# Kernel optimization log

Measured on AMD Instinct MI355X. Metric: run time of the kernel, lower is better.

## Reference

```python
import jax, jax.numpy as jnp
import numpy as np

N = 100_000          # nodes
DEG = 16             # avg degree (random edges)
E = N * DEG + N      # edges incl. self-loops (ensures no zero in-degree)
NFEAT = 256
NHID = 64
NHEADS = 8
NCLASS = 40
NEG_SLOPE = 0.2
S_F = 1.0
EPS = 1e-6


def setup_inputs() -> dict:
    key = jax.random.key(0)
    ks = jax.random.split(key, 12)
    x = jax.random.normal(ks[0], (N, NFEAT), dtype=jnp.float32)
    loops = jnp.arange(N, dtype=jnp.int32)
    src = jnp.concatenate([jax.random.randint(ks[1], (N * DEG,), 0, N, dtype=jnp.int32), loops])
    dst = jnp.concatenate([jax.random.randint(ks[2], (N * DEG,), 0, N, dtype=jnp.int32), loops])
    # layer-1: NHEADS independent single-head GATConv_G(nfeat -> nhid)
    W1 = (jax.random.normal(ks[3], (NHEADS, NHID, NFEAT), dtype=jnp.float32) * 0.05)
    al1 = jax.random.normal(ks[4], (NHEADS, NHID), dtype=jnp.float32) * 0.05
    ar1 = jax.random.normal(ks[5], (NHEADS, NHID), dtype=jnp.float32) * 0.05
    b1 = jnp.zeros((NHEADS, NHID), dtype=jnp.float32)
    p1 = jax.random.normal(ks[6], (NHEADS,), dtype=jnp.float32) * 0.1
    # layer-2: single-head GATConv_G(nhid*nheads -> nclass)
    W2 = jax.random.normal(ks[7], (NCLASS, NHID * NHEADS), dtype=jnp.float32) * 0.05
    al2 = jax.random.normal(ks[8], (NCLASS,), dtype=jnp.float32) * 0.05
    ar2 = jax.random.normal(ks[9], (NCLASS,), dtype=jnp.float32) * 0.05
    b2 = jnp.zeros((NCLASS,), dtype=jnp.float32)
    p2 = jax.random.normal(ks[10], (), dtype=jnp.float32) * 0.1
    return dict(x=x, src=src, dst=dst, W1=W1, al1=al1, ar1=ar1, b1=b1, p1=p1,
                W2=W2, al2=al2, ar2=ar2, b2=b2, p2=p2)


def _leaky_relu(x):
    return jnp.where(x >= 0, x, NEG_SLOPE * x)


def _edge_softmax(e, dst):
    # softmax over incoming edges of each destination node
    m = jax.ops.segment_max(e, dst, num_segments=N)
    ex = jnp.exp(e - m[dst])
    s = jax.ops.segment_sum(ex, dst, num_segments=N)
    return ex / s[dst]


def _gat_g_head(x, src, dst, W, al, ar, b, p):
    """One GATConv_G with num_heads=1. x:[N,Fin], W:[Fout,Fin] -> [N,Fout]."""
    ft = x @ W.T                                   # [N,Fout]
    el = ft @ al                                   # [N]
    er = ft @ ar                                   # [N]
    e = _leaky_relu(el[src] + er[dst])             # [E]
    a = _edge_softmax(e, dst)                      # [E]
    pe = jax.nn.sigmoid(p) + S_F                   # scalar, nonlinear-aggregation exponent
    mu = ft.min()                                  # global min (shift to make base positive)
    pf = jnp.power(ft - mu + EPS, pe)              # [N,Fout]
    msg = pf[src] * a[:, None]                     # [E,Fout] (u_mul_e)
    agg = jax.ops.segment_sum(msg, dst, num_segments=N)   # sum aggregation
    rst = jnp.power(agg + EPS, 1.0 / pe) + mu      # generalized-mean inverse
    return rst + b                                 # bias [Fout]


def reference(x, src, dst, W1, al1, ar1, b1, p1, W2, al2, ar2, b2, p2):
    # layer 1: NHEADS single-head GATConv_G, each with concat=True => elu, then concat
    heads = []
    for h in range(NHEADS):  # small fixed loop over structurally distinct heads
        heads.append(jax.nn.elu(_gat_g_head(x, src, dst, W1[h], al1[h], ar1[h], b1[h], p1[h])))
    hcat = jnp.concatenate(heads, axis=-1)         # [N, NHEADS*NHID]
    # layer 2: output GATConv_G (concat=False), then log_softmax classifier head
    out = _gat_g_head(hcat, src, dst, W2, al2, ar2, b2, p2)   # [N, NCLASS]
    return jax.nn.log_softmax(out, axis=-1)
```

## Files before the change

### kernel.cpp

```cpp
#include <hip/hip_runtime.h>

#define NN 100000
#define EE 1700000
#define F1 256
#define NH 8
#define HF 64
#define C1 512
#define C2 40
#define EPS 1e-6f

#define OF_PF1   ((size_t)0)
#define OF_HCAT  (OF_PF1  + 102400000ULL)
#define OF_FT2   (OF_HCAT + 102400000ULL)
#define OF_EL1   (OF_FT2  + 16000000ULL)
#define OF_ER1   (OF_EL1  + 3200000ULL)
#define OF_EL2   (OF_ER1  + 3200000ULL)
#define OF_ER2   (OF_EL2  + 400000ULL)
#define OF_DEG   (OF_ER2  + 400000ULL)
#define OF_OFFS  (OF_DEG  + 400000ULL)
#define OF_CUR   (OF_OFFS + 400128ULL)
#define OF_SRCC  (OF_CUR  + 400000ULL)
#define OF_BSUM  (OF_SRCC + 6800000ULL)
#define OF_BOFF  (OF_BSUM + 2048ULL)
#define OF_PRM   (OF_BOFF + 2048ULL)
#define OF_XH    (OF_HCAT)
#define OF_WH    (OF_HCAT + 51200000ULL)


typedef _Float16 f16x8 __attribute__((ext_vector_type(8)));
typedef _Float16 f16x4 __attribute__((ext_vector_type(4)));
typedef float f32x4 __attribute__((ext_vector_type(4)));

__device__ __forceinline__ unsigned f2key(float f){
  unsigned u = __float_as_uint(f);
  return (u & 0x80000000u) ? ~u : (u | 0x80000000u);
}
__device__ __forceinline__ float key2f(unsigned k){
  unsigned u = (k & 0x80000000u) ? (k & 0x7FFFFFFFu) : ~k;
  return __uint_as_float(u);
}
__device__ __forceinline__ unsigned short f2b(float f){
  unsigned u = __float_as_uint(f);
  unsigned r = u + 0x7FFFu + ((u >> 16) & 1u);
  return (unsigned short)(r >> 16);
}
__device__ __forceinline__ float b2f(unsigned short b){
  return __uint_as_float(((unsigned)b) << 16);
}
__device__ __forceinline__ float leaky(float e){ return e >= 0.f ? e : 0.2f*e; }

__device__ __forceinline__ void gload16(const _Float16* g, char* l){
  __builtin_amdgcn_global_load_lds((const __attribute__((address_space(1))) void*)g,
                                   (__attribute__((address_space(3))) void*)l, 16, 0, 0);
}

__global__ void k_init(const float* __restrict__ p1, const float* __restrict__ p2, unsigned* __restrict__ prm){
  int t = threadIdx.x;
  float* prf = (float*)prm;
  if (t < 8){
    prm[t] = 0xFFFFFFFFu;
    float pe = 1.f/(1.f + __expf(-p1[t])) + 1.0f;
    prf[16 + t] = pe;
    prf[24 + t] = 1.f/pe;
  }
  if (t == 0){
    prm[8] = 0xFFFFFFFFu;
    float pe = 1.f/(1.f + __expf(-p2[0])) + 1.0f;
    prf[32] = pe;
    prf[33] = 1.f/pe;
  }
}

__global__ void k_zero_deg(int* __restrict__ deg){
  int i = blockIdx.x*256 + threadIdx.x;
  if (i < NN) deg[i] = 0;
}

__global__ void k_cvt16(const float* __restrict__ in, _Float16* __restrict__ out){
  int i = blockIdx.x*256 + threadIdx.x;
  const float4* p = (const float4*)in + (size_t)i*2;
  float4 a = p[0], b = p[1];
  f16x8 h = {(_Float16)a.x,(_Float16)a.y,(_Float16)a.z,(_Float16)a.w,
             (_Float16)b.x,(_Float16)b.y,(_Float16)b.z,(_Float16)b.w};
  *((f16x8*)out + i) = h;
}

#define G1_BM 128
#define G1_BN 128
#define G1_BK 64
__global__ __launch_bounds__(256) void k_gemm1(const _Float16* __restrict__ xh, const _Float16* __restrict__ Wh,
                                               unsigned short* __restrict__ ft1b, unsigned* __restrict__ prm){
  __shared__ __align__(16) char smem[35840];
  char* Abase = smem;
  char* Bbase = smem + 16384;
  unsigned short (*Cs)[136] = (unsigned short (*)[136])smem;

  int t = threadIdx.x;
  int lane = t & 63, w = t >> 6;
  int wr = w >> 1, wc = w & 1;
  int ct = blockIdx.x * G1_BN;
  int rt = blockIdx.y * G1_BM;

  int lr8 = lane >> 3;
  int gcs = (lane & 7) ^ lr8;

  f32x4 zero = {0.f,0.f,0.f,0.f};
  f32x4 acc[4][4];
  #pragma unroll
  for (int m=0;m<4;m++)
    #pragma unroll
    for (int n=0;n<4;n++) acc[m][n] = zero;

  for (int kt = 0; kt < F1; kt += G1_BK){
    #pragma unroll
    for (int i = 0; i < 4; i++){
      int ch = w*4 + i;
      int row = ch*8 + lr8;
      int ga = min(rt + row, NN-1);
      gload16(xh + (size_t)ga*F1 + kt + gcs*8, Abase + ch*1024);
      gload16(Wh + (size_t)(ct+row)*F1 + kt + gcs*8, Bbase + ch*1024);
    }
    __syncthreads();
    #pragma unroll
    for (int kk = 0; kk < 2; kk++){
      f16x8 af[4], bf[4];
      #pragma unroll
      for (int m=0;m<4;m++){
        int row = wr*64 + m*16 + (lane & 15);
        int g = kk*4 + (lane >> 4);
        af[m] = *(f16x8*)(Abase + ((row*8 + (g ^ (row & 7)))<<4));
      }
      #pragma unroll
      for (int n=0;n<4;n++){
        int row = wc*64 + n*16 + (lane & 15);
        int g = kk*4 + (lane >> 4);
        bf[n] = *(f16x8*)(Bbase + ((row*8 + (g ^ (row & 7)))<<4));
      }
      #pragma unroll
      for (int m=0;m<4;m++)
        #pragma unroll
        for (int n=0;n<4;n++)
          acc[m][n] = __builtin_amdgcn_mfma_f32_16x16x32_f16(af[m], bf[n], acc[m][n], 0, 0, 0);
    }
    __syncthreads();
  }

  int h = (ct >> 6) + wc;
  unsigned kmin = 0xFFFFFFFFu;
  #pragma unroll
  for (int m=0;m<4;m++){
    #pragma unroll
    for (int n=0;n<4;n++){
      int cl = wc*64 + n*16 + (lane & 15);
      int rl = wr*64 + m*16 + (lane >> 4)*4;
      #pragma unroll
      for (int j=0;j<4;j++){
        unsigned short ub = f2b(acc[m][n][j]);
        Cs[rl + j][cl] = ub;
        kmin = min(kmin, f2key(b2f(ub)));
      }
    }
  }
  #pragma unroll
  for (int off=1; off<64; off<<=1) kmin = min(kmin, (unsigned)__shfl_xor((int)kmin, off));
  if (lane == 0) atomicMin(&prm[h], kmin);
  __syncthreads();

  #pragma unroll
  for (int p = 0; p < 8; p++){
    int flat = p*256 + t;
    int row = flat >> 4;
    int q   = flat & 15;
    int gr = rt + row;
    if (gr < NN){
      uint4 v = *(const uint4*)&Cs[row][q*8];
      *(uint4*)&ft1b[(size_t)gr*C1 + ct + q*8] = v;
    }
  }
}

__global__ void k_count(const int* __restrict__ dst, int* __restrict__ deg){
  int e = blockIdx.x*256 + threadIdx.x;
  if (e < EE) atomicAdd(&deg[dst[e]], 1);
}
__global__ void k_scan1(const int* __restrict__ deg, int* __restrict__ offs, int* __restrict__ bsum){
  __shared__ int s[256];
  int t = threadIdx.x; int i = blockIdx.x*256 + t;
  int v = (i < NN) ? deg[i] : 0;
  s[t] = v; __syncthreads();
  for (int off=1; off<256; off<<=1){
    int tmp = (t>=off) ? s[t-off] : 0;
    __syncthreads(); s[t] += tmp; __syncthreads();
  }
  if (i < NN) offs[i] = s[t] - v;
  if (t == 255) bsum[blockIdx.x] = s[255];
}
__global__ void k_scan2(int* __restrict__ bsum, int* __restrict__ boff, int nb){
  __shared__ int s[512];
  int t = threadIdx.x;
  int v = (t < nb) ? bsum[t] : 0;
  s[t] = v; __syncthreads();
  for (int off=1; off<512; off<<=1){
    int tmp = (t>=off) ? s[t-off] : 0;
    __syncthreads(); s[t] += tmp; __syncthreads();
  }
  if (t < nb) boff[t] = s[t] - v;
}
__global__ void k_scan3(int* __restrict__ offs, int* __restrict__ cur, const int* __restrict__ boff){
  int i = blockIdx.x*256 + threadIdx.x;
  if (i < NN){
    int v = offs[i] + boff[blockIdx.x];
    offs[i] = v; cur[i] = v;
  }
  if (i == 0) offs[NN] = EE;
}
__global__ void k_fill(const int* __restrict__ src, const int* __restrict__ dst,
                       int* __restrict__ cur, int* __restrict__ srcc){
  int e = blockIdx.x*256 + threadIdx.x;
  if (e < EE){
    int d = dst[e];
    int pos = atomicAdd(&cur[d], 1);
    srcc[pos] = src[e];
  }
}

__global__ __launch_bounds__(256) void k_transform1(unsigned short* __restrict__ ft1b,
    const float* __restrict__ al1, const float* __restrict__ ar1,
    float* __restrict__ el1, float* __restrict__ er1, const unsigned* __restrict__ prm){
  int lane = threadIdx.x & 63; int w = threadIdx.x >> 6;
  int n = blockIdx.x*4 + w;
  if (n >= NN) return;
  const float* prf = (const float*)prm;
  float vv[8], elp[8], erp[8];
  #pragma unroll
  for (int h=0; h<8; h++){
    vv[h]  = b2f(ft1b[(size_t)n*C1 + h*HF + lane]);
    elp[h] = vv[h]*al1[h*HF + lane];
    erp[h] = vv[h]*ar1[h*HF + lane];
  }
  #pragma unroll
  for (int h=0; h<8; h++){
    #pragma unroll
    for (int off=1; off<64; off<<=1){
      elp[h] += __shfl_xor(elp[h], off);
      erp[h] += __shfl_xor(erp[h], off);
    }
  }
  if (lane == 0){
    #pragma unroll
    for (int h=0; h<8; h++){ el1[(size_t)n*8+h]=elp[h]; er1[(size_t)n*8+h]=erp[h]; }
  }
  #pragma unroll
  for (int h=0; h<8; h++){
    float mu = key2f(prm[h]);
    float pe = prf[16+h];
    float base = vv[h] - mu + EPS;
    ft1b[(size_t)n*C1 + h*HF + lane] = f2b(__expf(pe * __logf(base)));
  }
}

__global__ __launch_bounds__(256) void k_agg1(const unsigned short* __restrict__ pf1b,
    const float* __restrict__ el1, const float* __restrict__ er1,
    const int* __restrict__ offs, const int* __restrict__ srcc,
    const float* __restrict__ b1, const unsigned* __restrict__ prm,
    _Float16* __restrict__ hcath){
  int lane = threadIdx.x & 63; int w = threadIdx.x >> 6;
  int v = blockIdx.x*4 + w;
  if (v >= NN) return;
  const float* prf = (const float*)prm;
  int h = lane >> 3;
  int s = lane & 7;
  int start = offs[v], end = offs[v+1];
  float erh = er1[(size_t)v*8 + h];

  float m = -INFINITY;
  for (int pos = start + s; pos < end; pos += 8){
    int u = srcc[pos];
    float e = leaky(el1[(size_t)u*8 + h] + erh);
    m = fmaxf(m, e);
  }
  m = fmaxf(m, __shfl_xor(m,1)); m = fmaxf(m, __shfl_xor(m,2)); m = fmaxf(m, __shfl_xor(m,4));
  float S = 0.f;
  for (int pos = start + s; pos < end; pos += 8){
    int u = srcc[pos];
    float e = leaky(el1[(size_t)u*8 + h] + erh);
    S += __expf(e - m);
  }
  S += __shfl_xor(S,1); S += __shfl_xor(S,2); S += __shfl_xor(S,4);
  float invS = 1.f / S;

  int es = lane >> 5;
  int hc = (lane >> 2) & 7;
  int q4 = lane & 3;
  float mh    = __shfl(m,    hc*8);
  float invSh = __shfl(invS, hc*8);
  float erhc  = __shfl(erh,  hc*8);

  float acc[16];
  #pragma unroll
  for (int j=0;j<16;j++) acc[j]=0.f;
  for (int pos = start + es; pos < end; pos += 2){
    int u = srcc[pos];
    float e = leaky(el1[(size_t)u*8 + hc] + erhc);
    float a = __expf(e - mh) * invSh;
    const unsigned short* pr = &pf1b[(size_t)u*C1 + hc*HF + q4*16];
    uint4 qa = *(const uint4*)pr;
    uint4 qb = *(const uint4*)(pr + 8);
    acc[0]  += a*b2f((unsigned short)(qa.x & 0xFFFFu));
    acc[1]  += a*b2f((unsigned short)(qa.x >> 16));
    acc[2]  += a*b2f((unsigned short)(qa.y & 0xFFFFu));
    acc[3]  += a*b2f((unsigned short)(qa.y >> 16));
    acc[4]  += a*b2f((unsigned short)(qa.z & 0xFFFFu));
    acc[5]  += a*b2f((unsigned short)(qa.z >> 16));
    acc[6]  += a*b2f((unsigned short)(qa.w & 0xFFFFu));
    acc[7]  += a*b2f((unsigned short)(qa.w >> 16));
    acc[8]  += a*b2f((unsigned short)(qb.x & 0xFFFFu));
    acc[9]  += a*b2f((unsigned short)(qb.x >> 16));
    acc[10] += a*b2f((unsigned short)(qb.y & 0xFFFFu));
    acc[11] += a*b2f((unsigned short)(qb.y >> 16));
    acc[12] += a*b2f((unsigned short)(qb.z & 0xFFFFu));
    acc[13] += a*b2f((unsigned short)(qb.z >> 16));
    acc[14] += a*b2f((unsigned short)(qb.w & 0xFFFFu));
    acc[15] += a*b2f((unsigned short)(qb.w >> 16));
  }
  #pragma unroll
  for (int j=0;j<16;j++) acc[j] += __shfl_xor(acc[j], 32);

  float mu = key2f(prm[hc]);
  float ipe = prf[24+hc];
  int fb = q4*16 + es*8;
  f16x8 o;
  #pragma unroll
  for (int j=0;j<8;j++){
    float r = __expf(ipe * __logf(acc[es*8 + j] + EPS)) + mu + b1[hc*HF + fb + j];
    o[j] = (_Float16)((r > 0.f) ? r : (__expf(r) - 1.f));
  }
  *(f16x8*)&hcath[(size_t)v*C1 + hc*HF + fb] = o;
}

#define G2_BM 64
#define G2_BK 64
__global__ __launch_bounds__(256) void k_gemm2(const _Float16* __restrict__ hcath, const float* __restrict__ W2,
    float* __restrict__ ft2, float* __restrict__ el2, float* __restrict__ er2,
    const float* __restrict__ al2, const float* __restrict__ ar2, unsigned* __restrict__ prm){
  __shared__ float As[G2_BK][G2_BM];
  __shared__ float Bs[G2_BK][C2];
  __shared__ float els[64], ers[64];
  __shared__ unsigned mk;
  int t = threadIdx.x;
  int tx = t & 7, ty = t >> 3;
  int rt = blockIdx.x * G2_BM;
  float acc[2][5];
  #pragma unroll
  for (int i=0;i<2;i++)
    #pragma unroll
    for (int j=0;j<5;j++) acc[i][j]=0.f;

  for (int k0=0; k0<C1; k0+=G2_BK){
    #pragma unroll
    for (int i=0;i<2;i++){
      int id = t*2 + i;
      int row = id >> 3; int c8 = (id & 7)*8;
      int gr = rt + row;
      f16x8 q = {0,0,0,0,0,0,0,0};
      if (gr < NN) q = *(const f16x8*)&hcath[(size_t)gr*C1 + k0 + c8];
      #pragma unroll
      for (int j=0;j<8;j++) As[c8+j][row] = (float)q[j];
    }
    #pragma unroll
    for (int i=0;i<10;i++){
      int id = t + i*256;
      int c = id >> 6, kk = id & 63;
      Bs[kk][c] = W2[(size_t)c*C1 + k0 + kk];
    }
    __syncthreads();
    #pragma unroll
    for (int kk=0; kk<G2_BK; ++kk){
      float2 a = *(float2*)&As[kk][ty*2];
      float b0=Bs[kk][tx*5+0], b1v=Bs[kk][tx*5+1], b2v=Bs[kk][tx*5+2], b3v=Bs[kk][tx*5+3], b4v=Bs[kk][tx*5+4];
      acc[0][0]+=a.x*b0; acc[0][1]+=a.x*b1v; acc[0][2]+=a.x*b2v; acc[0][3]+=a.x*b3v; acc[0][4]+=a.x*b4v;
      acc[1][0]+=a.y*b0; acc[1][1]+=a.y*b1v; acc[1][2]+=a.y*b2v; acc[1][3]+=a.y*b3v; acc[1][4]+=a.y*b4v;
    }
    __syncthreads();
  }

  if (t < 64){ els[t]=0.f; ers[t]=0.f; }
  if (t == 0) mk = 0xFFFFFFFFu;
  __syncthreads();
  unsigned kmin = 0xFFFFFFFFu;
  #pragma unroll
  for (int i=0;i<2;i++){
    int r = rt + ty*2 + i;
    if (r < NN){
      float elp=0.f, erp=0.f;
      #pragma unroll
      for (int j=0;j<5;j++){
        float vv = acc[i][j]; int c = tx*5+j;
        ft2[(size_t)r*C2 + c] = vv;
        elp += vv*al2[c]; erp += vv*ar2[c];
        kmin = min(kmin, f2key(vv));
      }
      atomicAdd(&els[ty*2+i], elp);
      atomicAdd(&ers[ty*2+i], erp);
    }
  }
  atomicMin(&mk, kmin);
  __syncthreads();
  if (t < 64 && rt + t < NN){ el2[rt+t]=els[t]; er2[rt+t]=ers[t]; }
  if (t == 0) atomicMin(&prm[8], mk);
}

__global__ void k_transform2(float* __restrict__ ft2, const unsigned* __restrict__ prm){
  int i = blockIdx.x*256 + threadIdx.x;
  if (i >= NN*C2) return;
  const float* prf = (const float*)prm;
  float mu = key2f(prm[8]);
  float pe = prf[32];
  float v = ft2[i];
  ft2[i] = __expf(pe * __logf(v - mu + EPS));
}

__global__ __launch_bounds__(256) void k_agg2(const float* __restrict__ pf2,
    const float* __restrict__ el2, const float* __restrict__ er2,
    const int* __restrict__ offs, const int* __restrict__ srcc,
    const float* __restrict__ b2, const unsigned* __restrict__ prm,
    float* __restrict__ out){
  int lane = threadIdx.x & 63; int w = threadIdx.x >> 6;
  int v = blockIdx.x*4 + w;
  if (v >= NN) return;
  const float* prf = (const float*)prm;
  int start = offs[v], end = offs[v+1];
  float erv = er2[v];

  float m = -INFINITY;
  for (int pos = start + lane; pos < end; pos += 64){
    float e = leaky(el2[srcc[pos]] + erv);
    m = fmaxf(m, e);
  }
  #pragma unroll
  for (int off=1; off<64; off<<=1) m = fmaxf(m, __shfl_xor(m, off));
  float S = 0.f;
  for (int pos = start + lane; pos < end; pos += 64){
    float e = leaky(el2[srcc[pos]] + erv);
    S += __expf(e - m);
  }
  #pragma unroll
  for (int off=1; off<64; off<<=1) S += __shfl_xor(S, off);
  float invS = 1.f / S;

  int s = lane >> 4;
  int c = lane & 15;
  float a0=0.f, a1=0.f, a2=0.f, a3=0.f;
  for (int pos = start + s; pos < end; pos += 4){
    int u = srcc[pos];
    float a = __expf(leaky(el2[u] + erv) - m) * invS;
    if (c < 10){
      float4 q = *(const float4*)&pf2[(size_t)u*C2 + c*4];
      a0 += a*q.x; a1 += a*q.y; a2 += a*q.z; a3 += a*q.w;
    }
  }
  a0 += __shfl_xor(a0,16); a1 += __shfl_xor(a1,16); a2 += __shfl_xor(a2,16); a3 += __shfl_xor(a3,16);
  a0 += __shfl_xor(a0,32); a1 += __shfl_xor(a1,32); a2 += __shfl_xor(a2,32); a3 += __shfl_xor(a3,32);

  float y[4];
  float mx;
  if (c < 10){
    float mu = key2f(prm[8]);
    float ipe = prf[33];
    float av[4] = {a0,a1,a2,a3};
    #pragma unroll
    for (int j=0;j<4;j++) y[j] = __expf(ipe * __logf(av[j] + EPS)) + mu + b2[c*4 + j];
    mx = fmaxf(fmaxf(y[0],y[1]), fmaxf(y[2],y[3]));
  } else {
    y[0]=y[1]=y[2]=y[3]=-INFINITY;
    mx = -INFINITY;
  }
  mx = fmaxf(mx, __shfl_xor(mx,1)); mx = fmaxf(mx, __shfl_xor(mx,2));
  mx = fmaxf(mx, __shfl_xor(mx,4)); mx = fmaxf(mx, __shfl_xor(mx,8));
  float se = 0.f;
  if (c < 10){
    #pragma unroll
    for (int j=0;j<4;j++) se += __expf(y[j] - mx);
  }
  se += __shfl_xor(se,1); se += __shfl_xor(se,2); se += __shfl_xor(se,4); se += __shfl_xor(se,8);
  float ls = __logf(se);
  if (s == 0 && c < 10){
    float4 o = make_float4(y[0]-mx-ls, y[1]-mx-ls, y[2]-mx-ls, y[3]-mx-ls);
    *(float4*)&out[(size_t)v*C2 + c*4] = o;
  }
}

extern "C" void kernel_launch(void* const* d_in, const int* in_sizes, int n_in,
                              void* d_out, int out_size, void* d_ws, size_t ws_size,
                              hipStream_t stream){
  const float* x   = (const float*)d_in[0];
  const int*   src = (const int*)d_in[1];
  const int*   dst = (const int*)d_in[2];
  const float* W1  = (const float*)d_in[3];
  const float* al1 = (const float*)d_in[4];
  const float* ar1 = (const float*)d_in[5];
  const float* b1  = (const float*)d_in[6];
  const float* p1  = (const float*)d_in[7];
  const float* W2  = (const float*)d_in[8];
  const float* al2 = (const float*)d_in[9];
  const float* ar2 = (const float*)d_in[10];
  const float* b2  = (const float*)d_in[11];
  const float* p2  = (const float*)d_in[12];
  float* out = (float*)d_out;
  char* ws = (char*)d_ws;

  unsigned short* pf1b  = (unsigned short*)(ws + OF_PF1);
  _Float16* hcath = (_Float16*)(ws + OF_HCAT);
  _Float16* xh  = (_Float16*)(ws + OF_XH);
  _Float16* Wh  = (_Float16*)(ws + OF_WH);
  float* ft2   = (float*)(ws + OF_FT2);
  float* el1   = (float*)(ws + OF_EL1);
  float* er1   = (float*)(ws + OF_ER1);
  float* el2   = (float*)(ws + OF_EL2);
  float* er2   = (float*)(ws + OF_ER2);
  int*   deg   = (int*)(ws + OF_DEG);
  int*   offs  = (int*)(ws + OF_OFFS);
  int*   cur   = (int*)(ws + OF_CUR);
  int*   srcc  = (int*)(ws + OF_SRCC);
  int*   bsum  = (int*)(ws + OF_BSUM);
  int*   boff  = (int*)(ws + OF_BOFF);
  unsigned* prm = (unsigned*)(ws + OF_PRM);

  const int NB1 = (NN + 255)/256;
  const int NBE = (EE + 255)/256;

  k_init<<<1, 64, 0, stream>>>(p1, p2, prm);
  k_zero_deg<<<NB1, 256, 0, stream>>>(deg);
  k_cvt16<<<12500, 256, 0, stream>>>(x, xh);
  k_cvt16<<<64, 256, 0, stream>>>(W1, Wh);
  k_gemm1<<<dim3(C1/G1_BN, (NN + G1_BM - 1)/G1_BM), 256, 0, stream>>>(xh, Wh, pf1b, prm);
  k_count<<<NBE, 256, 0, stream>>>(dst, deg);
  k_scan1<<<NB1, 256, 0, stream>>>(deg, offs, bsum);
  k_scan2<<<1, 512, 0, stream>>>(bsum, boff, NB1);
  k_scan3<<<NB1, 256, 0, stream>>>(offs, cur, boff);
  k_fill<<<NBE, 256, 0, stream>>>(src, dst, cur, srcc);
  k_transform1<<<NN/4, 256, 0, stream>>>(pf1b, al1, ar1, el1, er1, prm);
  k_agg1<<<NN/4, 256, 0, stream>>>(pf1b, el1, er1, offs, srcc, b1, prm, hcath);
  k_gemm2<<<(NN + G2_BM - 1)/G2_BM, 256, 0, stream>>>(hcath, W2, ft2, el2, er2, al2, ar2, prm);
  k_transform2<<<(NN*C2 + 255)/256, 256, 0, stream>>>(ft2, prm);
  k_agg2<<<NN/4, 256, 0, stream>>>(ft2, el2, er2, offs, srcc, b2, prm, out);
}
```

Before: 1.014 ms.

## Rewrite layer-2 GEMM with fp16 MFMA and swizzled LDS tiles

Replaces the scalar fp32 FMA layer-2 GEMM (hcat x W2^T) with an MFMA 16x16x32 f16 kernel on 128-row tiles. W2 is padded to 48 rows and converted to fp16 by a new small kernel. Operand tiles are loaded into LDS with an XOR swizzle to avoid bank conflicts. The el/er reductions move from LDS atomics to wave shuffles. The aim is to cut the compute-bound cost of the second GEMM, at the price of fp16 rounding on W2 and one extra launch.

```diff
diff --git a/kernel.cpp b/kernel.cpp
--- a/kernel.cpp
+++ b/kernel.cpp
@@ -23,6 +23,7 @@
 #define OF_BSUM  (OF_SRCC + 6800000ULL)
 #define OF_BOFF  (OF_BSUM + 2048ULL)
 #define OF_PRM   (OF_BOFF + 2048ULL)
+#define OF_W2H   (OF_PRM  + 1024ULL)
 #define OF_XH    (OF_HCAT)
 #define OF_WH    (OF_HCAT + 51200000ULL)
 
@@ -83,6 +84,12 @@
   f16x8 h = {(_Float16)a.x,(_Float16)a.y,(_Float16)a.z,(_Float16)a.w,
              (_Float16)b.x,(_Float16)b.y,(_Float16)b.z,(_Float16)b.w};
   *((f16x8*)out + i) = h;
+}
+
+__global__ void k_cvtW2(const float* __restrict__ W2, _Float16* __restrict__ W2h){
+  int i = blockIdx.x*256 + threadIdx.x;
+  int row = i >> 9, col = i & 511;
+  W2h[i] = (row < C2) ? (_Float16)W2[row*C1 + col] : (_Float16)0.f;
 }
 
 #define G1_BM 128
@@ -338,75 +345,103 @@
   *(f16x8*)&hcath[(size_t)v*C1 + hc*HF + fb] = o;
 }
 
-#define G2_BM 64
-#define G2_BK 64
-__global__ __launch_bounds__(256) void k_gemm2(const _Float16* __restrict__ hcath, const float* __restrict__ W2,
+__global__ __launch_bounds__(256) void k_gemm2(const _Float16* __restrict__ hcath, const _Float16* __restrict__ W2h,
     float* __restrict__ ft2, float* __restrict__ el2, float* __restrict__ er2,
     const float* __restrict__ al2, const float* __restrict__ ar2, unsigned* __restrict__ prm){
-  __shared__ float As[G2_BK][G2_BM];
-  __shared__ float Bs[G2_BK][C2];
-  __shared__ float els[64], ers[64];
+  __shared__ __align__(16) char smem[45056];
+  char* Abase = smem;
+  char* Bbase = smem + 32768;
   __shared__ unsigned mk;
   int t = threadIdx.x;
-  int tx = t & 7, ty = t >> 3;
-  int rt = blockIdx.x * G2_BM;
-  float acc[2][5];
-  #pragma unroll
-  for (int i=0;i<2;i++)
-    #pragma unroll
-    for (int j=0;j<5;j++) acc[i][j]=0.f;
-
-  for (int k0=0; k0<C1; k0+=G2_BK){
-    #pragma unroll
-    for (int i=0;i<2;i++){
-      int id = t*2 + i;
-      int row = id >> 3; int c8 = (id & 7)*8;
-      int gr = rt + row;
-      f16x8 q = {0,0,0,0,0,0,0,0};
-      if (gr < NN) q = *(const f16x8*)&hcath[(size_t)gr*C1 + k0 + c8];
-      #pragma unroll
-      for (int j=0;j<8;j++) As[c8+j][row] = (float)q[j];
-    }
-    #pragma unroll
-    for (int i=0;i<10;i++){
-      int id = t + i*256;
-      int c = id >> 6, kk = id & 63;
-      Bs[kk][c] = W2[(size_t)c*C1 + k0 + kk];
+  int lane = t & 63, w = t >> 6;
+  int rt = blockIdx.x * 128;
+  if (t == 0) mk = 0xFFFFFFFFu;
+
+  f32x4 zero = {0.f,0.f,0.f,0.f};
+  f32x4 acc[2][3];
+  #pragma unroll
+  for (int m=0;m<2;m++)
+    #pragma unroll
+    for (int n=0;n<3;n++) acc[m][n] = zero;
+
+  for (int step = 0; step < 4; step++){
+    #pragma unroll
+    for (int p = 0; p < 8; p++){
+      int idx = p*256 + t;
+      int row = idx >> 4, g = idx & 15;
+      int ga = min(rt + row, NN-1);
+      gload16(hcath + (size_t)ga*C1 + step*128 + ((g ^ (row & 7))<<3), Abase + idx*16);
+    }
+    #pragma unroll
+    for (int p = 0; p < 3; p++){
+      int idx = p*256 + t;
+      int row = idx >> 4, g = idx & 15;
+      gload16(W2h + (size_t)row*C1 + step*128 + ((g ^ (row & 7))<<3), Bbase + idx*16);
     }
     __syncthreads();
     #pragma unroll
-    for (int kk=0; kk<G2_BK; ++kk){
-      float2 a = *(float2*)&As[kk][ty*2];
-      float b0=Bs[kk][tx*5+0], b1v=Bs[kk][tx*5+1], b2v=Bs[kk][tx*5+2], b3v=Bs[kk][tx*5+3], b4v=Bs[kk][tx*5+4];
-      acc[0][0]+=a.x*b0; acc[0][1]+=a.x*b1v; acc[0][2]+=a.x*b2v; acc[0][3]+=a.x*b3v; acc[0][4]+=a.x*b4v;
-      acc[1][0]+=a.y*b0; acc[1][1]+=a.y*b1v; acc[1][2]+=a.y*b2v; acc[1][3]+=a.y*b3v; acc[1][4]+=a.y*b4v;
+    for (int kk = 0; kk < 4; kk++){
+      f16x8 af[2], bf[3];
+      #pragma unroll
+      for (int m=0;m<2;m++){
+        int row = w*32 + m*16 + (lane & 15);
+        int g = kk*4 + (lane >> 4);
+        af[m] = *(f16x8*)(Abase + ((row*16 + (g ^ (row & 7)))<<4));
+      }
+      #pragma unroll
+      for (int n=0;n<3;n++){
+        int row = n*16 + (lane & 15);
+        int g = kk*4 + (lane >> 4);
+        bf[n] = *(f16x8*)(Bbase + ((row*16 + (g ^ (row & 7)))<<4));
+      }
+      #pragma unroll
+      for (int m=0;m<2;m++)
+        #pragma unroll
+        for (int n=0;n<3;n++)
+          acc[m][n] = __builtin_amdgcn_mfma_f32_16x16x32_f16(af[m], bf[n], acc[m][n], 0, 0, 0);
     }
     __syncthreads();
   }
 
-  if (t < 64){ els[t]=0.f; ers[t]=0.f; }
-  if (t == 0) mk = 0xFFFFFFFFu;
+  int c0 = lane & 15;
+  unsigned kmin = 0xFFFFFFFFu;
+  #pragma unroll
+  for (int m=0;m<2;m++){
+    float elp[4] = {0.f,0.f,0.f,0.f};
+    float erp[4] = {0.f,0.f,0.f,0.f};
+    #pragma unroll
+    for (int n=0;n<3;n++){
+      int col = n*16 + c0;
+      bool okc = (col < C2);
+      float alc = okc ? al2[col] : 0.f;
+      float arc = okc ? ar2[col] : 0.f;
+      int rbase = rt + w*32 + m*16 + (lane >> 4)*4;
+      #pragma unroll
+      for (int j=0;j<4;j++){
+        float vv = acc[m][n][j];
+        int row = rbase + j;
+        if (okc && row < NN){
+          ft2[(size_t)row*C2 + col] = vv;
+          elp[j] += vv*alc; erp[j] += vv*arc;
+          kmin = min(kmin, f2key(vv));
+        }
+      }
+    }
+    #pragma unroll
+    for (int j=0;j<4;j++){
+      #pragma unroll
+      for (int off=1; off<16; off<<=1){
+        elp[j] += __shfl_xor(elp[j], off);
+        erp[j] += __shfl_xor(erp[j], off);
+      }
+      int row = rt + w*32 + m*16 + (lane >> 4)*4 + j;
+      if (c0 == 0 && row < NN){ el2[row] = elp[j]; er2[row] = erp[j]; }
+    }
+  }
+  #pragma unroll
+  for (int off=1; off<64; off<<=1) kmin = min(kmin, (unsigned)__shfl_xor((int)kmin, off));
+  if (lane == 0) atomicMin(&mk, kmin);
   __syncthreads();
-  unsigned kmin = 0xFFFFFFFFu;
-  #pragma unroll
-  for (int i=0;i<2;i++){
-    int r = rt + ty*2 + i;
-    if (r < NN){
-      float elp=0.f, erp=0.f;
-      #pragma unroll
-      for (int j=0;j<5;j++){
-        float vv = acc[i][j]; int c = tx*5+j;
-        ft2[(size_t)r*C2 + c] = vv;
-        elp += vv*al2[c]; erp += vv*ar2[c];
-        kmin = min(kmin, f2key(vv));
-      }
-      atomicAdd(&els[ty*2+i], elp);
-      atomicAdd(&ers[ty*2+i], erp);
-    }
-  }
-  atomicMin(&mk, kmin);
-  __syncthreads();
-  if (t < 64 && rt + t < NN){ el2[rt+t]=els[t]; er2[rt+t]=ers[t]; }
   if (t == 0) atomicMin(&prm[8], mk);
 }
 
@@ -513,6 +548,7 @@
   _Float16* hcath = (_Float16*)(ws + OF_HCAT);
   _Float16* xh  = (_Float16*)(ws + OF_XH);
   _Float16* Wh  = (_Float16*)(ws + OF_WH);
+  _Float16* W2h = (_Float16*)(ws + OF_W2H);
   float* ft2   = (float*)(ws + OF_FT2);
   float* el1   = (float*)(ws + OF_EL1);
   float* er1   = (float*)(ws + OF_ER1);
@@ -533,6 +569,7 @@
   k_zero_deg<<<NB1, 256, 0, stream>>>(deg);
   k_cvt16<<<12500, 256, 0, stream>>>(x, xh);
   k_cvt16<<<64, 256, 0, stream>>>(W1, Wh);
+  k_cvtW2<<<96, 256, 0, stream>>>(W2, W2h);
   k_gemm1<<<dim3(C1/G1_BN, (NN + G1_BM - 1)/G1_BM), 256, 0, stream>>>(xh, Wh, pf1b, prm);
   k_count<<<NBE, 256, 0, stream>>>(dst, deg);
   k_scan1<<<NB1, 256, 0, stream>>>(deg, offs, bsum);
@@ -541,7 +578,7 @@
   k_fill<<<NBE, 256, 0, stream>>>(src, dst, cur, srcc);
   k_transform1<<<NN/4, 256, 0, stream>>>(pf1b, al1, ar1, el1, er1, prm);
   k_agg1<<<NN/4, 256, 0, stream>>>(pf1b, el1, er1, offs, srcc, b1, prm, hcath);
-  k_gemm2<<<(NN + G2_BM - 1)/G2_BM, 256, 0, stream>>>(hcath, W2, ft2, el2, er2, al2, ar2, prm);
+  k_gemm2<<<(NN + 127)/128, 256, 0, stream>>>(hcath, W2h, ft2, el2, er2, al2, ar2, prm);
   k_transform2<<<(NN*C2 + 255)/256, 256, 0, stream>>>(ft2, prm);
   k_agg2<<<NN/4, 256, 0, stream>>>(ft2, el2, er2, offs, srcc, b2, prm, out);
 }
```

Result: faster. 896.8 us (-11.5%).
